# Kernel optimization log

Hardware: AMD Instinct MI355X
Metric: run time of the kernel (lower is better)

The kernel has to match this reference:

```python
import jax, jax.numpy as jnp
import numpy as np

CUTOFF = 5.0
MAX_NBR = 32      # max_num_neighbors
LOOP = True
B, M = 128, 1024  # molecules, atoms per molecule (batch is uniform: batch[i] = i // M)
BOX = 26.0        # box side chosen so ~30 atoms fall within CUTOFF


def setup_inputs() -> dict:
    key = jax.random.key(0)
    pos = jax.random.uniform(key, (B * M, 3), dtype=jnp.float32) * BOX
    batch = jnp.repeat(jnp.arange(B, dtype=jnp.int32), M)
    return {"pos": pos, "batch": batch}


def reference(pos, batch):
    # radius_graph with per-graph (molecule) candidate search. Equal-size
    # molecules (batch = arange // M) let us use a dense [B, M, M] candidate
    # matrix per molecule; truncation keeps the K nearest within cutoff
    # (PyG keeps an arbitrary K within cutoff; nearest-K is the deterministic
    # variant). Output has fixed shape [2, B*M*K] padded with self-loops.
    posb = pos.reshape(B, M, 3)
    sq = jnp.sum(posb * posb, axis=-1)                       # [B, M]
    dot = jnp.einsum('bmd,bnd->bmn', posb, posb)             # [B, M, M]
    d2 = jnp.maximum(sq[:, :, None] + sq[:, None, :] - 2.0 * dot, 0.0)
    within = d2 <= CUTOFF * CUTOFF
    if not LOOP:
        within = within & ~jnp.eye(M, dtype=bool)[None]
    neg = jnp.where(within, -d2, -jnp.inf)
    vals, idx = jax.lax.top_k(neg, MAX_NBR)                  # [B, M, K]
    valid = jnp.isfinite(vals)
    center = jnp.arange(M, dtype=idx.dtype)[None, :, None]   # [1, M, 1]
    idx_eff = jnp.where(valid, idx, center)                  # pad invalid -> self

    b_ix = jnp.arange(B)[:, None, None]
    nbr = posb[b_ix, idx_eff]                                # [B, M, K, 3]
    edge_vec = nbr - posb[:, :, None, :]                     # pos[src] - pos[dst]

    is_self = idx_eff == center
    wmask = valid & ~is_self                                 # self-loops get weight 0
    d2sel = jnp.sum(edge_vec * edge_vec, axis=-1)
    edge_weight = jnp.where(wmask, jnp.sqrt(jnp.where(wmask, d2sel, 1.0)), 0.0)

    offs = (jnp.arange(B, dtype=idx.dtype) * M)[:, None, None]
    src = (offs + idx_eff).reshape(-1)                       # neighbor (edge_index[0])
    dst = jnp.broadcast_to(offs + center, (B, M, MAX_NBR)).reshape(-1)
    edge_index = jnp.stack([src, dst])                       # [2, B*M*K]
    return edge_index, edge_weight.reshape(-1), edge_vec.reshape(-1, 3)
```

## Files before the change

### kernel.cpp

```cpp
#include <hip/hip_runtime.h>

#define NB 128
#define NM 1024
#define NK 32
#define NQ 4
#define NS 12
#define CUT2 25.0f
#define CUT2_BITS 0x41C80000u
#define KEYMASK   0xFFFFFC00u

typedef unsigned int   u32;
typedef unsigned short u16;
typedef float vf4 __attribute__((ext_vector_type(4)));

__global__ __launch_bounds__(256) void pack_atoms(const float* __restrict__ pos,
                                                  float4* __restrict__ scanb)
{
  int i = blockIdx.x * 256 + threadIdx.x;
  float x = pos[3*i+0], y = pos[3*i+1], z = pos[3*i+2];
  float sq = x*x + y*y + z*z;
  scanb[i] = make_float4(-2.f*x, -2.f*y, -2.f*z, sq);
}

__device__ __forceinline__ void ce_asc(u32 &a, u32 &b) {
  u32 mn = a < b ? a : b;
  u32 mx = a < b ? b : a;
  a = mn; b = mx;
}

template <int N, int K, int D>
__device__ __forceinline__ void bitonic_pass(u32* r) {
#pragma unroll
  for (int i = 0; i < N; ++i)
    if ((i & D) == 0) {
      if ((i & K) == 0) ce_asc(r[i], r[i | D]);
      else              ce_asc(r[i | D], r[i]);
    }
}

__global__ __launch_bounds__(256, 5) void radius_knn(const float4* __restrict__ scanb,
                                                     float* __restrict__ out)
{
  __shared__ float4 s4[NM];
  __shared__ u32 lmem[4096];
  u16* lists = (u16*)lmem;

  const int tid     = threadIdx.x;
  const int ctr     = tid & 63;
  const int quarter = tid >> 6;
  const int molb    = blockIdx.x & 127;
  const int grp     = blockIdx.x >> 7;
  const int c       = molb * NM + grp * 64 + ctr;
  const int mloc    = c & (NM - 1);

  const float4* st = scanb + (size_t)molb * NM;
  for (int t = tid; t < NM; t += 256) s4[t] = st[t];
  __syncthreads();

  const float4 mc = s4[mloc];
  const float mex = -0.5f * mc.x, mey = -0.5f * mc.y, mez = -0.5f * mc.z;
  const float mew = mc.w;

  const float4* mp = scanb + ((size_t)(c >> 10) << 10);
  const int jbase = quarter * 256;
  int cnt = 0;
  float4 ta[4], tb[4];
#pragma unroll
  for (int u = 0; u < 4; ++u) ta[u] = mp[jbase + u];
  __builtin_amdgcn_sched_barrier(0);

  auto body = [&](const float4* t, int j0) {
#pragma unroll
    for (int u = 0; u < 4; ++u) {
      float d2 = __builtin_fmaf(mex, t[u].x,
                 __builtin_fmaf(mey, t[u].y,
                 __builtin_fmaf(mez, t[u].z, mew + t[u].w)));
      int slot = cnt < NS ? cnt : (NS - 1);
      lists[slot * 256 + tid] = (u16)(j0 + u);
      cnt += (d2 <= CUT2) ? 1 : 0;
    }
  };

  for (int g = 0; g < 64; g += 2) {
    const int j1 = jbase + (((g + 1) & 63) << 2);
#pragma unroll
    for (int u = 0; u < 4; ++u) tb[u] = mp[j1 + u];
    __builtin_amdgcn_sched_barrier(0);
    body(ta, jbase + (g << 2));
    const int j2 = jbase + (((g + 2) & 63) << 2);
#pragma unroll
    for (int u = 0; u < 4; ++u) ta[u] = mp[j2 + u];
    __builtin_amdgcn_sched_barrier(0);
    body(tb, jbase + ((g + 1) << 2));
  }
  if (cnt > NS) cnt = NS;

  const u32 PADK = 0x7F800000u | (u32)mloc;
  u32 r[32];
#pragma unroll
  for (int k = 0; k < 16; ++k) {
    u32 key = PADK;
    if (k < cnt) {
      int j = lists[k * 256 + tid];
      float4 cj = s4[j];
      float d2 = fmaxf(__builtin_fmaf(mex, cj.x,
                  __builtin_fmaf(mey, cj.y,
                  __builtin_fmaf(mez, cj.z, mew + cj.w))), 0.f);
      key = (__float_as_uint(d2) & KEYMASK) | (u32)j;
    }
    r[k] = key;
  }
  bitonic_pass<16, 2, 1>(r);
  bitonic_pass<16, 4, 2>(r); bitonic_pass<16, 4, 1>(r);
  bitonic_pass<16, 8, 4>(r); bitonic_pass<16, 8, 2>(r); bitonic_pass<16, 8, 1>(r);
  bitonic_pass<16,16, 8>(r); bitonic_pass<16,16, 4>(r); bitonic_pass<16,16, 2>(r); bitonic_pass<16,16, 1>(r);

  __syncthreads();
  {
    u32* myp = lmem + quarter * 1024 + ctr * 16;
#pragma unroll
    for (int k = 0; k < 16; ++k) myp[(k + ctr) & 15] = r[k];
  }
  __syncthreads();
  {
    u32* op = lmem + (quarter ^ 1) * 1024 + ctr * 16;
#pragma unroll
    for (int i = 0; i < 16; ++i) r[16 + i] = op[((15 - i) + ctr) & 15];
  }
  bitonic_pass<32,32,16>(r); bitonic_pass<32,32, 8>(r); bitonic_pass<32,32, 4>(r);
  bitonic_pass<32,32, 2>(r); bitonic_pass<32,32, 1>(r);

  __syncthreads();
  const int pairId = quarter >> 1;
  if ((quarter & 1) == 0) {
    u32* pp = lmem + pairId * 2048 + ctr * 32;
#pragma unroll
    for (int k = 0; k < 32; ++k) pp[(k + ctr) & 31] = r[k];
  }
  __syncthreads();
  {
    u32* opp = lmem + (1 - pairId) * 2048 + ctr * 32;
#pragma unroll
    for (int t = 0; t < 32; ++t) {
      u32 v = opp[((31 - t) + ctr) & 31];
      r[t] = r[t] < v ? r[t] : v;
    }
  }
  bitonic_pass<32,32,16>(r); bitonic_pass<32,32, 8>(r); bitonic_pass<32,32, 4>(r);
  bitonic_pass<32,32, 2>(r); bitonic_pass<32,32, 1>(r);

  const long long E = (long long)NB * NM * NK;
  const float base = (float)((c >> 10) * NM);
  const float nmex = -mex, nmey = -mey, nmez = -mez;

  if (quarter == 0) {
    vf4* ps = (vf4*)(out       + (size_t)c * NK);
    vf4* pd = (vf4*)(out +   E + (size_t)c * NK);
    const float fc = (float)c;
    const vf4 dstv = {fc, fc, fc, fc};
#pragma unroll
    for (int q = 0; q < 8; ++q) {
      float sv[4];
#pragma unroll
      for (int u = 0; u < 4; ++u) sv[u] = base + (float)(int)(r[4*q + u] & 1023u);
      ps[q] = (vf4){sv[0], sv[1], sv[2], sv[3]};
      pd[q] = dstv;
    }
  } else if (quarter == 1) {
    vf4* pw = (vf4*)(out + 2*E + (size_t)c * NK);
#pragma unroll
    for (int q = 0; q < 8; ++q) {
      float wv[4];
#pragma unroll
      for (int u = 0; u < 4; ++u) {
        u32 key = r[4*q + u];
        int idx = (int)(key & 1023u);
        float4 cj = s4[idx];
        bool valid = (key & KEYMASK) <= CUT2_BITS;
        float vx = __builtin_fmaf(-0.5f, cj.x, nmex);
        float vy = __builtin_fmaf(-0.5f, cj.y, nmey);
        float vz = __builtin_fmaf(-0.5f, cj.z, nmez);
        bool wm  = valid && (idx != mloc);
        float d2s = vx*vx + vy*vy + vz*vz;
        wv[u] = wm ? sqrtf(d2s) : 0.0f;
      }
      pw[q] = (vf4){wv[0], wv[1], wv[2], wv[3]};
    }
  } else if (quarter == 2) {
    vf4* pv = (vf4*)(out + 3*E + (size_t)c * NK * 3);
#pragma unroll
    for (int q = 0; q < 4; ++q) {
      float vv[12];
#pragma unroll
      for (int u = 0; u < 4; ++u) {
        int idx = (int)(r[4*q + u] & 1023u);
        float4 cj = s4[idx];
        vv[3*u+0] = __builtin_fmaf(-0.5f, cj.x, nmex);
        vv[3*u+1] = __builtin_fmaf(-0.5f, cj.y, nmey);
        vv[3*u+2] = __builtin_fmaf(-0.5f, cj.z, nmez);
      }
      pv[3*q+0] = (vf4){vv[0], vv[1], vv[2],  vv[3]};
      pv[3*q+1] = (vf4){vv[4], vv[5], vv[6],  vv[7]};
      pv[3*q+2] = (vf4){vv[8], vv[9], vv[10], vv[11]};
    }
  } else {
    vf4* pv = (vf4*)(out + 3*E + (size_t)c * NK * 3) + 12;
#pragma unroll
    for (int q = 0; q < 4; ++q) {
      float vv[12];
#pragma unroll
      for (int u = 0; u < 4; ++u) {
        int idx = (int)(r[16 + 4*q + u] & 1023u);
        float4 cj = s4[idx];
        vv[3*u+0] = __builtin_fmaf(-0.5f, cj.x, nmex);
        vv[3*u+1] = __builtin_fmaf(-0.5f, cj.y, nmey);
        vv[3*u+2] = __builtin_fmaf(-0.5f, cj.z, nmez);
      }
      pv[3*q+0] = (vf4){vv[0], vv[1], vv[2],  vv[3]};
      pv[3*q+1] = (vf4){vv[4], vv[5], vv[6],  vv[7]};
      pv[3*q+2] = (vf4){vv[8], vv[9], vv[10], vv[11]};
    }
  }
}

extern "C" void kernel_launch(void* const* d_in, const int* in_sizes, int n_in,
                              void* d_out, int out_size, void* d_ws, size_t ws_size,
                              hipStream_t stream) {
  const float* pos = (const float*)d_in[0];
  float* out = (float*)d_out;
  float4* scanb = (float4*)d_ws;
  hipLaunchKernelGGL(pack_atoms, dim3((NB*NM)/256), dim3(256), 0, stream, pos, scanb);
  hipLaunchKernelGGL(radius_knn, dim3(NB * (NM / 64)), dim3(256), 0, stream,
                     scanb, out);
}
```

Measured before the change: 187.0 us.

## Bin atoms into a spatial cell grid and scan only neighbouring cells

The packing kernel becomes a per-molecule counting sort of atoms into a 5x5x5 cell grid. It stores sorted packed coordinates, the original atom ids and the cell start offsets. The search kernel builds a flat candidate list from the cells around each 64-atom group's bounding box, replacing the brute-force scan over all 1024 atoms. This cuts distance evaluations and frees the shared position buffer, which allows higher occupancy. In exchange it adds an extra indirection to map sorted indices back to original ids, and nearest-neighbour ties may be broken in a different order.

```diff
diff --git a/kernel.cpp b/kernel.cpp
--- a/kernel.cpp
+++ b/kernel.cpp
@@ -3,23 +3,62 @@
 #define NB 128
 #define NM 1024
 #define NK 32
-#define NQ 4
 #define NS 12
 #define CUT2 25.0f
 #define CUT2_BITS 0x41C80000u
 #define KEYMASK   0xFFFFFC00u
+#define INV_CELL  (1.0f/5.2f)
+#define NCELL3    125
 
 typedef unsigned int   u32;
 typedef unsigned short u16;
 typedef float vf4 __attribute__((ext_vector_type(4)));
 
-__global__ __launch_bounds__(256) void pack_atoms(const float* __restrict__ pos,
-                                                  float4* __restrict__ scanb)
+__global__ __launch_bounds__(256) void pack_bin(const float* __restrict__ pos,
+                                                float4* __restrict__ sortedg,
+                                                u16* __restrict__ origid,
+                                                u16* __restrict__ startsg)
 {
-  int i = blockIdx.x * 256 + threadIdx.x;
-  float x = pos[3*i+0], y = pos[3*i+1], z = pos[3*i+2];
-  float sq = x*x + y*y + z*z;
-  scanb[i] = make_float4(-2.f*x, -2.f*y, -2.f*z, sq);
+  __shared__ u32 hist[NCELL3 + 1];
+  __shared__ u32 starts[NCELL3 + 1];
+  __shared__ u32 cur[NCELL3];
+  const int tid = threadIdx.x;
+  const int mb  = blockIdx.x;
+  if (tid <= NCELL3) hist[tid] = 0;
+  __syncthreads();
+
+  float xx[4], yy[4], zz[4];
+  int cid[4];
+#pragma unroll
+  for (int k = 0; k < 4; ++k) {
+    int i  = k * 256 + tid;
+    int gi = mb * NM + i;
+    float x = pos[3*gi+0], y = pos[3*gi+1], z = pos[3*gi+2];
+    xx[k] = x; yy[k] = y; zz[k] = z;
+    int cx = (int)(x * INV_CELL); cx = cx > 4 ? 4 : cx;
+    int cy = (int)(y * INV_CELL); cy = cy > 4 ? 4 : cy;
+    int cz = (int)(z * INV_CELL); cz = cz > 4 ? 4 : cz;
+    cid[k] = (cz * 5 + cy) * 5 + cx;
+    atomicAdd(&hist[cid[k]], 1u);
+  }
+  __syncthreads();
+  if (tid == 0) {
+    u32 run = 0;
+    for (int i = 0; i < NCELL3; ++i) { starts[i] = run; run += hist[i]; }
+    starts[NCELL3] = run;
+  }
+  __syncthreads();
+  if (tid <= NCELL3) startsg[mb*(NCELL3+1) + tid] = (u16)starts[tid];
+  if (tid <  NCELL3) cur[tid] = starts[tid];
+  __syncthreads();
+#pragma unroll
+  for (int k = 0; k < 4; ++k) {
+    int i = k * 256 + tid;
+    u32 p = atomicAdd(&cur[cid[k]], 1u);
+    float x = xx[k], y = yy[k], z = zz[k];
+    sortedg[mb*NM + p] = make_float4(-2.f*x, -2.f*y, -2.f*z, x*x + y*y + z*z);
+    origid[mb*NM + p]  = (u16)i;
+  }
 }
 
 __device__ __forceinline__ void ce_asc(u32 &a, u32 &b) {
@@ -38,71 +77,116 @@
     }
 }
 
-__global__ __launch_bounds__(256, 5) void radius_knn(const float4* __restrict__ scanb,
+__global__ __launch_bounds__(256, 8) void radius_knn(const float4* __restrict__ sortedg,
+                                                     const u16* __restrict__ origg,
+                                                     const u16* __restrict__ startsg,
                                                      float* __restrict__ out)
 {
-  __shared__ float4 s4[NM];
   __shared__ u32 lmem[4096];
-  u16* lists = (u16*)lmem;
+  __shared__ u16 orig_s[NM];
+  u16* lists  = (u16*)lmem;
+  u32* rowbuf = lmem + 1536;
+  u16* flat   = (u16*)(lmem + 1568);
+  u16* st_s   = (u16*)(lmem + 2112);
 
   const int tid     = threadIdx.x;
   const int ctr     = tid & 63;
   const int quarter = tid >> 6;
   const int molb    = blockIdx.x & 127;
   const int grp     = blockIdx.x >> 7;
-  const int c       = molb * NM + grp * 64 + ctr;
-  const int mloc    = c & (NM - 1);
-
-  const float4* st = scanb + (size_t)molb * NM;
-  for (int t = tid; t < NM; t += 256) s4[t] = st[t];
-  __syncthreads();
-
-  const float4 mc = s4[mloc];
-  const float mex = -0.5f * mc.x, mey = -0.5f * mc.y, mez = -0.5f * mc.z;
+  const int spos    = grp * 64 + ctr;
+  const int molbase = molb * NM;
+
+  for (int t = tid; t < NM; t += 256) orig_s[t] = origg[molbase + t];
+  if (tid <= NCELL3) st_s[tid] = startsg[molb*(NCELL3+1) + tid];
+
+  const float4 mc  = sortedg[molbase + spos];
+  const int   mloc = origg[molbase + spos];
+  const float mex = -0.5f*mc.x, mey = -0.5f*mc.y, mez = -0.5f*mc.z;
   const float mew = mc.w;
-
-  const float4* mp = scanb + ((size_t)(c >> 10) << 10);
-  const int jbase = quarter * 256;
+  const int c = molbase + mloc;
+
+  int cx = (int)(mex * INV_CELL); cx = cx > 4 ? 4 : cx;
+  int cy = (int)(mey * INV_CELL); cy = cy > 4 ? 4 : cy;
+  int cz = (int)(mez * INV_CELL); cz = cz > 4 ? 4 : cz;
+  int mnx = cx, mxx = cx, mny = cy, mxy = cy, mnz = cz, mxz = cz;
+#pragma unroll
+  for (int m = 32; m; m >>= 1) {
+    mnx = min(mnx, __shfl_xor(mnx, m, 64)); mxx = max(mxx, __shfl_xor(mxx, m, 64));
+    mny = min(mny, __shfl_xor(mny, m, 64)); mxy = max(mxy, __shfl_xor(mxy, m, 64));
+    mnz = min(mnz, __shfl_xor(mnz, m, 64)); mxz = max(mxz, __shfl_xor(mxz, m, 64));
+  }
+  __syncthreads();
+
+  if (quarter == 0) {
+    const int zlo = max(mnz-1, 0), zhi = min(mxz+1, 4);
+    const int ylo = max(mny-1, 0), yhi = min(mxy+1, 4);
+    const int xlo = max(mnx-1, 0), xhi = min(mxx+1, 4);
+    const int rz = ctr / 5, ry = ctr % 5;
+    int czc = zlo + rz, cyc = ylo + ry;
+    u32 rs = 0, len = 0;
+    if (ctr < 25 && czc <= zhi && cyc <= yhi) {
+      int rowb = (czc*5 + cyc)*5;
+      rs  = st_s[rowb + xlo];
+      u32 re = st_s[rowb + xhi + 1];
+      len = re - rs;
+    }
+    u32 incl = len;
+#pragma unroll
+    for (int d = 1; d < 32; d <<= 1) {
+      u32 t = __shfl_up(incl, d, 64);
+      if (ctr >= d) incl += t;
+    }
+    if (ctr < 25)  rowbuf[ctr] = (rs << 16) | (incl - len);
+    if (ctr == 24) { rowbuf[25] = incl; lmem[1563] = incl; }
+  }
+  __syncthreads();
+
+  const int C  = (int)lmem[1563];
+  const int C4 = (C + 15) & ~15;
+  for (int p = tid; p < C; p += 256) {
+    int r = 0;
+    while (p >= (int)(rowbuf[r+1] & 0xFFFFu)) ++r;
+    u32 e = rowbuf[r];
+    int j = (int)(e >> 16) + (p - (int)(e & 0xFFFFu));
+    flat[(p & 3) * 264 + (p >> 2)] = (u16)j;
+  }
+  for (int p = C + tid; p < C4; p += 256) flat[(p & 3) * 264 + (p >> 2)] = 0xFFFFu;
+  __syncthreads();
+
   int cnt = 0;
-  float4 ta[4], tb[4];
-#pragma unroll
-  for (int u = 0; u < 4; ++u) ta[u] = mp[jbase + u];
-  __builtin_amdgcn_sched_barrier(0);
-
-  auto body = [&](const float4* t, int j0) {
-#pragma unroll
-    for (int u = 0; u < 4; ++u) {
-      float d2 = __builtin_fmaf(mex, t[u].x,
-                 __builtin_fmaf(mey, t[u].y,
-                 __builtin_fmaf(mez, t[u].z, mew + t[u].w)));
-      int slot = cnt < NS ? cnt : (NS - 1);
-      lists[slot * 256 + tid] = (u16)(j0 + u);
-      cnt += (d2 <= CUT2) ? 1 : 0;
-    }
-  };
-
-  for (int g = 0; g < 64; g += 2) {
-    const int j1 = jbase + (((g + 1) & 63) << 2);
-#pragma unroll
-    for (int u = 0; u < 4; ++u) tb[u] = mp[j1 + u];
-    __builtin_amdgcn_sched_barrier(0);
-    body(ta, jbase + (g << 2));
-    const int j2 = jbase + (((g + 2) & 63) << 2);
-#pragma unroll
-    for (int u = 0; u < 4; ++u) ta[u] = mp[j2 + u];
-    __builtin_amdgcn_sched_barrier(0);
-    body(tb, jbase + ((g + 1) << 2));
+  const u16* fl = flat + quarter * 264;
+  const int T = C4 >> 4;
+  for (int g = 0; g < T; ++g) {
+    uint2 jj = *((const uint2*)(fl + 4*g));
+    int j0 = jj.x & 0xFFFF, j1 = jj.x >> 16;
+    int j2 = jj.y & 0xFFFF, j3 = jj.y >> 16;
+    float4 c0 = sortedg[molbase + (j0 & 1023)];
+    float4 c1 = sortedg[molbase + (j1 & 1023)];
+    float4 c2 = sortedg[molbase + (j2 & 1023)];
+    float4 c3 = sortedg[molbase + (j3 & 1023)];
+#define PROC(cj, jv)                                                        \
+    {                                                                       \
+      float d2 = __builtin_fmaf(mex, cj.x, __builtin_fmaf(mey, cj.y,        \
+                 __builtin_fmaf(mez, cj.z, mew + cj.w)));                   \
+      d2 = (jv < 1024) ? d2 : 1.0e30f;                       \
+      int slot = cnt < NS ? cnt : (NS - 1);                                 \
+      lists[slot * 256 + tid] = (u16)(jv & 1023);                           \
+      cnt += (d2 <= CUT2) ? 1 : 0;                                          \
+    }
+    PROC(c0, j0) PROC(c1, j1) PROC(c2, j2) PROC(c3, j3)
+#undef PROC
   }
   if (cnt > NS) cnt = NS;
 
-  const u32 PADK = 0x7F800000u | (u32)mloc;
+  const u32 PADK = 0x7F800000u | (u32)spos;
   u32 r[32];
 #pragma unroll
   for (int k = 0; k < 16; ++k) {
     u32 key = PADK;
     if (k < cnt) {
       int j = lists[k * 256 + tid];
-      float4 cj = s4[j];
+      float4 cj = sortedg[molbase + j];
       float d2 = fmaxf(__builtin_fmaf(mex, cj.x,
                   __builtin_fmaf(mey, cj.y,
                   __builtin_fmaf(mez, cj.z, mew + cj.w))), 0.f);
@@ -150,7 +234,7 @@
   bitonic_pass<32,32, 2>(r); bitonic_pass<32,32, 1>(r);
 
   const long long E = (long long)NB * NM * NK;
-  const float base = (float)((c >> 10) * NM);
+  const float base = (float)molbase;
   const float nmex = -mex, nmey = -mey, nmez = -mez;
 
   if (quarter == 0) {
@@ -162,7 +246,10 @@
     for (int q = 0; q < 8; ++q) {
       float sv[4];
 #pragma unroll
-      for (int u = 0; u < 4; ++u) sv[u] = base + (float)(int)(r[4*q + u] & 1023u);
+      for (int u = 0; u < 4; ++u) {
+        int idx = (int)(r[4*q + u] & 1023u);
+        sv[u] = base + (float)orig_s[idx];
+      }
       ps[q] = (vf4){sv[0], sv[1], sv[2], sv[3]};
       pd[q] = dstv;
     }
@@ -175,12 +262,12 @@
       for (int u = 0; u < 4; ++u) {
         u32 key = r[4*q + u];
         int idx = (int)(key & 1023u);
-        float4 cj = s4[idx];
+        float4 cj = sortedg[molbase + idx];
         bool valid = (key & KEYMASK) <= CUT2_BITS;
         float vx = __builtin_fmaf(-0.5f, cj.x, nmex);
         float vy = __builtin_fmaf(-0.5f, cj.y, nmey);
         float vz = __builtin_fmaf(-0.5f, cj.z, nmez);
-        bool wm  = valid && (idx != mloc);
+        bool wm  = valid && (idx != spos);
         float d2s = vx*vx + vy*vy + vz*vz;
         wv[u] = wm ? sqrtf(d2s) : 0.0f;
       }
@@ -194,7 +281,7 @@
 #pragma unroll
       for (int u = 0; u < 4; ++u) {
         int idx = (int)(r[4*q + u] & 1023u);
-        float4 cj = s4[idx];
+        float4 cj = sortedg[molbase + idx];
         vv[3*u+0] = __builtin_fmaf(-0.5f, cj.x, nmex);
         vv[3*u+1] = __builtin_fmaf(-0.5f, cj.y, nmey);
         vv[3*u+2] = __builtin_fmaf(-0.5f, cj.z, nmez);
@@ -211,7 +298,7 @@
 #pragma unroll
       for (int u = 0; u < 4; ++u) {
         int idx = (int)(r[16 + 4*q + u] & 1023u);
-        float4 cj = s4[idx];
+        float4 cj = sortedg[molbase + idx];
         vv[3*u+0] = __builtin_fmaf(-0.5f, cj.x, nmex);
         vv[3*u+1] = __builtin_fmaf(-0.5f, cj.y, nmey);
         vv[3*u+2] = __builtin_fmaf(-0.5f, cj.z, nmez);
@@ -228,8 +315,11 @@
                               hipStream_t stream) {
   const float* pos = (const float*)d_in[0];
   float* out = (float*)d_out;
-  float4* scanb = (float4*)d_ws;
-  hipLaunchKernelGGL(pack_atoms, dim3((NB*NM)/256), dim3(256), 0, stream, pos, scanb);
+  float4* sortedg = (float4*)d_ws;
+  u16* origid  = (u16*)((char*)d_ws + (size_t)(2u << 20));
+  u16* startsg = (u16*)((char*)d_ws + (size_t)(2u << 20) + (256u << 10));
+  hipLaunchKernelGGL(pack_bin, dim3(NB), dim3(256), 0, stream,
+                     pos, sortedg, origid, startsg);
   hipLaunchKernelGGL(radius_knn, dim3(NB * (NM / 64)), dim3(256), 0, stream,
-                     scanb, out);
-}
+                     sortedg, origid, startsg, out);
+}
```

After: 193.2 us. 1.03x slower.
